# Optimization experiments

Hardware: AMD Instinct MI355X
Metric: run time of the kernel (lower is better)

The kernel has to match this reference:

```python
import jax, jax.numpy as jnp
import numpy as np

N_NODES = 100000
N_EDGES = 1600000
DIMS = [128, 128, 128, 64]


def setup_inputs() -> dict:
    key = jax.random.key(0)
    ks = jax.random.split(key, 12)
    inp = {
        "features": jax.random.normal(ks[0], (N_NODES, DIMS[0]), dtype=jnp.float32),
        "src": jax.random.randint(ks[1], (N_EDGES,), 0, N_NODES, dtype=jnp.int64),
        "dst": jax.random.randint(ks[2], (N_EDGES,), 0, N_NODES, dtype=jnp.int64),
        "edge_weight": jax.random.uniform(ks[3], (N_EDGES,), dtype=jnp.float32),
    }
    # GraphConv weights (xavier-like scale) and biases per layer
    for i in range(3):
        fin, fout = DIMS[i], DIMS[i + 1]
        scale = (2.0 / (fin + fout)) ** 0.5
        inp[f"W{i}"] = jax.random.normal(ks[4 + i], (fin, fout), dtype=jnp.float32) * scale
        inp[f"b{i}"] = jnp.zeros((fout,), dtype=jnp.float32)
    return inp


def _graph_conv(h, W, b, src, dst, ew, out_norm, in_norm):
    # DGL GraphConv, norm='both', with per-edge weight (u_mul_e message).
    fin, fout = W.shape
    h = h * out_norm[:, None]
    if fin > fout:  # mult W first to reduce message width
        h = h @ W
    msg = h[src] * ew[:, None]                       # [E, d] irregular gather
    agg = jax.ops.segment_sum(msg, dst, num_segments=N_NODES)
    agg = agg * in_norm[:, None]
    if fin <= fout:
        agg = agg @ W
    return agg + b


def reference(features, src, dst, edge_weight, W0, b0, W1, b1, W2, b2):
    ones = jnp.ones((N_EDGES,), dtype=features.dtype)
    out_deg = jax.ops.segment_sum(ones, src, num_segments=N_NODES)
    in_deg = jax.ops.segment_sum(ones, dst, num_segments=N_NODES)
    out_norm = jnp.clip(out_deg, 1.0, None) ** -0.5
    in_norm = jnp.clip(in_deg, 1.0, None) ** -0.5
    h = features
    Ws = [(W0, b0), (W1, b1), (W2, b2)]
    for i, (W, b) in enumerate(Ws):
        h = _graph_conv(h, W, b, src, dst, edge_weight, out_norm, in_norm)
        if i < len(Ws) - 1:
            h = jax.nn.relu(h)
    return h
```

## Files before the change

kernel.cpp:

```cpp
#include <hip/hip_runtime.h>
#include <cstddef>
#include <cstdint>

typedef float f4 __attribute__((ext_vector_type(4)));
typedef unsigned long long u64;
typedef unsigned short u16;
typedef unsigned short u16x8 __attribute__((ext_vector_type(8)));
typedef short short8 __attribute__((ext_vector_type(8)));

__device__ __forceinline__ u64 ldnt8(const void* p) {
    return __builtin_nontemporal_load((const u64*)(p));
}
__device__ __forceinline__ u16 bfrn(float f) {
    unsigned u = __float_as_uint(f);
    return (u16)((u + 0x7FFFu + ((u >> 16) & 1u)) >> 16);
}
__device__ __forceinline__ float bl(unsigned w) { return __uint_as_float(w << 16); }
__device__ __forceinline__ float bh(unsigned w) { return __uint_as_float(w & 0xFFFF0000u); }


#define EPB 4096

__global__ void __launch_bounds__(256)
k_p1(const int* __restrict__ src, const int* __restrict__ dst,
     u16* __restrict__ lrank_s, u16* __restrict__ lrank_d,
     int* __restrict__ bh_s, int* __restrict__ bh_d, int NB, int E) {
    __shared__ int hs[512], hd[512];
    const int t = threadIdx.x, b = blockIdx.x;
    for (int i = t; i < NB; i += 256) { hs[i] = 0; hd[i] = 0; }
    __syncthreads();
    const int e0 = b * EPB;
    #pragma unroll
    for (int j = 0; j < 4; ++j) {
        const int e = e0 + j * 1024 + t * 4;
        if (e + 4 <= E) {
            const int4 d = *(const int4*)&dst[e];
            const int4 s = *(const int4*)&src[e];
            unsigned rd0 = atomicAdd(&hd[d.x >> 8], 1);
            unsigned rd1 = atomicAdd(&hd[d.y >> 8], 1);
            unsigned rd2 = atomicAdd(&hd[d.z >> 8], 1);
            unsigned rd3 = atomicAdd(&hd[d.w >> 8], 1);
            unsigned rs0 = atomicAdd(&hs[s.x >> 8], 1);
            unsigned rs1 = atomicAdd(&hs[s.y >> 8], 1);
            unsigned rs2 = atomicAdd(&hs[s.z >> 8], 1);
            unsigned rs3 = atomicAdd(&hs[s.w >> 8], 1);
            *(uint2*)&lrank_d[e] = make_uint2(rd0 | (rd1 << 16), rd2 | (rd3 << 16));
            *(uint2*)&lrank_s[e] = make_uint2(rs0 | (rs1 << 16), rs2 | (rs3 << 16));
        } else {
            for (int k = e; k < E && k < e + 4; ++k) {
                lrank_d[k] = (u16)atomicAdd(&hd[dst[k] >> 8], 1);
                lrank_s[k] = (u16)atomicAdd(&hs[src[k] >> 8], 1);
            }
        }
    }
    __syncthreads();
    for (int i = t; i < NB; i += 256) {
        bh_d[b * NB + i] = hd[i];
        bh_s[b * NB + i] = hs[i];
    }
}

__global__ void __launch_bounds__(512)
k_p2(int* __restrict__ bh_d, int* __restrict__ bh_s,
     int* __restrict__ cb_d, int* __restrict__ cb_s, int NB, int B1) {
    __shared__ int s[512];
    const int B = blockIdx.x, i = threadIdx.x;
    int* bh = blockIdx.y ? bh_s : bh_d;
    int* cb = blockIdx.y ? cb_s : cb_d;
    const int v = (i < B1) ? bh[i * NB + B] : 0;
    s[i] = v;
    __syncthreads();
    for (int off = 1; off < 512; off <<= 1) {
        const int x = (i >= off) ? s[i - off] : 0;
        __syncthreads();
        s[i] += x;
        __syncthreads();
    }
    if (i < B1) bh[i * NB + B] = s[i] - v;
    if (i == 511) cb[B] = s[511];
}

__global__ void __launch_bounds__(512)
k_p2b(const int* __restrict__ cb_d, const int* __restrict__ cb_s,
      int* __restrict__ bktb_d, int* __restrict__ bktb_s,
      int* __restrict__ row, int NB, int N, int E) {
    __shared__ int s[512];
    const int t = threadIdx.x;
    int v = (t < NB) ? cb_d[t] : 0;
    s[t] = v;
    __syncthreads();
    for (int off = 1; off < 512; off <<= 1) {
        const int x = (t >= off) ? s[t - off] : 0;
        __syncthreads();
        s[t] += x;
        __syncthreads();
    }
    if (t < NB) bktb_d[t] = s[t] - v;
    __syncthreads();
    v = (t < NB) ? cb_s[t] : 0;
    s[t] = v;
    __syncthreads();
    for (int off = 1; off < 512; off <<= 1) {
        const int x = (t >= off) ? s[t - off] : 0;
        __syncthreads();
        s[t] += x;
        __syncthreads();
    }
    if (t < NB) bktb_s[t] = s[t] - v;
    if (t == 0) row[N] = E;
}

__global__ void __launch_bounds__(256)
k_p3(const int* __restrict__ src, const int* __restrict__ dst,
     const float* __restrict__ ew,
     const u16* __restrict__ lrank_s, const u16* __restrict__ lrank_d,
     const int* __restrict__ bh_s, const int* __restrict__ bh_d,
     const int* __restrict__ bktb_s, const int* __restrict__ bktb_d,
     int* __restrict__ tdst, int2* __restrict__ tsw, int* __restrict__ tsrc,
     int NB, int E) {
    const int t = threadIdx.x, b = blockIdx.x;
    const int e0 = b * EPB;
    #pragma unroll
    for (int j = 0; j < 4; ++j) {
        const int e = e0 + j * 1024 + t * 4;
        if (e + 4 <= E) {
            const int4 d = *(const int4*)&dst[e];
            const int4 s = *(const int4*)&src[e];
            const f4   w = *(const f4*)&ew[e];
            const uint2 rd = *(const uint2*)&lrank_d[e];
            const uint2 rs = *(const uint2*)&lrank_s[e];
            const int dd[4] = {d.x, d.y, d.z, d.w};
            const int ss[4] = {s.x, s.y, s.z, s.w};
            const float ww[4] = {w.x, w.y, w.z, w.w};
            const int rrd[4] = {(int)(rd.x & 0xFFFF), (int)(rd.x >> 16),
                                (int)(rd.y & 0xFFFF), (int)(rd.y >> 16)};
            const int rrs[4] = {(int)(rs.x & 0xFFFF), (int)(rs.x >> 16),
                                (int)(rs.y & 0xFFFF), (int)(rs.y >> 16)};
            #pragma unroll
            for (int k = 0; k < 4; ++k) {
                const int Bd = dd[k] >> 8;
                const int posd = bktb_d[Bd] + bh_d[b * NB + Bd] + rrd[k];
                tdst[posd] = dd[k];
                tsw[posd] = make_int2(ss[k], __float_as_int(ww[k]));
                const int Bs = ss[k] >> 8;
                const int poss = bktb_s[Bs] + bh_s[b * NB + Bs] + rrs[k];
                tsrc[poss] = ss[k];
            }
        } else {
            for (int k = e; k < E && k < e + 4; ++k) {
                const int dv = dst[k], sv = src[k];
                const int Bd = dv >> 8;
                const int posd = bktb_d[Bd] + bh_d[b * NB + Bd] + (int)lrank_d[k];
                tdst[posd] = dv;
                tsw[posd] = make_int2(sv, __float_as_int(ew[k]));
                const int Bs = sv >> 8;
                const int poss = bktb_s[Bs] + bh_s[b * NB + Bs] + (int)lrank_s[k];
                tsrc[poss] = sv;
            }
        }
    }
}

__global__ void __launch_bounds__(256)
k_p4s(const int* __restrict__ tsrc, const int* __restrict__ bktb_s,
      const int* __restrict__ cb_s, float* __restrict__ onorm, int NB, int N) {
    __shared__ int cnt[256];
    const int B = blockIdx.x, t = threadIdx.x;
    cnt[t] = 0;
    __syncthreads();
    const int base = bktb_s[B], cb = cb_s[B];
    for (int i = t; i < cb; i += 256) atomicAdd(&cnt[tsrc[base + i] & 255], 1);
    __syncthreads();
    const int n = (B << 8) + t;
    if (n < N) {
        const int c = cnt[t];
        onorm[n] = rsqrtf((float)(c < 1 ? 1 : c));
    }
}

__global__ void __launch_bounds__(256)
k_p4d(const int* __restrict__ tdst, const int2* __restrict__ tsw,
      const int* __restrict__ bktb_d, const int* __restrict__ cb_d,
      const float* __restrict__ onorm, int* __restrict__ row,
      float* __restrict__ inorm, int2* __restrict__ csr, int NB, int N) {
    __shared__ int cnt[256], cnt2[256], lrow[256], sc[256];
    const int B = blockIdx.x, t = threadIdx.x;
    cnt[t] = 0; cnt2[t] = 0;
    __syncthreads();
    const int base = bktb_d[B], cb = cb_d[B];
    for (int i = t; i < cb; i += 256) atomicAdd(&cnt[tdst[base + i] & 255], 1);
    __syncthreads();
    const int v = cnt[t];
    sc[t] = v;
    __syncthreads();
    for (int off = 1; off < 256; off <<= 1) {
        const int x = (t >= off) ? sc[t - off] : 0;
        __syncthreads();
        sc[t] += x;
        __syncthreads();
    }
    const int excl = sc[t] - v;
    lrow[t] = excl;
    const int n = (B << 8) + t;
    if (n < N) {
        row[n] = base + excl;
        inorm[n] = rsqrtf((float)(v < 1 ? 1 : v));
    }
    __syncthreads();
    for (int i = t; i < cb; i += 256) {
        const int d = tdst[base + i] & 255;
        const int2 sw = tsw[base + i];
        const int r = atomicAdd(&cnt2[d], 1);
        const float coef = __int_as_float(sw.y) * onorm[sw.x];
        csr[base + lrow[d] + r] = make_int2(sw.x, __float_as_int(coef));
    }
}

__global__ void __launch_bounds__(256)
k_cvt(const float* __restrict__ in, u16* __restrict__ out, int n8) {
    const int i = blockIdx.x * blockDim.x + threadIdx.x;
    if (i < n8) {
        const f4 v0 = *(const f4*)(in + (size_t)i * 8);
        const f4 v1 = *(const f4*)(in + (size_t)i * 8 + 4);
        u16x8 r = {bfrn(v0.x), bfrn(v0.y), bfrn(v0.z), bfrn(v0.w),
                   bfrn(v1.x), bfrn(v1.y), bfrn(v1.z), bfrn(v1.w)};
        *(u16x8*)(out + (size_t)i * 8) = r;
    }
}

template <int LOGC>
__global__ void __launch_bounds__(256)
k_wcvt(const float* __restrict__ W, u16* __restrict__ Wt, int K) {
    const int idx = blockIdx.x * 256 + threadIdx.x;
    if (idx < (K << LOGC)) {
        const int k = idx >> LOGC;
        const int c = idx & ((1 << LOGC) - 1);
        Wt[(size_t)c * K + k] = bfrn(W[idx]);
    }
}

__global__ void __launch_bounds__(256)
k_agg128b(const u16* __restrict__ h, const int* __restrict__ row,
          const int2* __restrict__ csr, const float* __restrict__ inorm,
          u16* __restrict__ out, int N) {
    const int node = (int)((blockIdx.x * blockDim.x + threadIdx.x) >> 6);
    if (node >= N) return;
    const int lane = threadIdx.x & 63;
    const int q = lane >> 4;
    const int col = (lane & 15) * 8;
    int p = row[node];
    const int e = row[node + 1];
    float a0 = 0, a1 = 0, a2 = 0, a3 = 0, a4 = 0, a5 = 0, a6 = 0, a7 = 0;
    for (; p + 16 <= e; p += 16) {
        const u64 c0 = ldnt8(&csr[p + q]);
        const u64 c1 = ldnt8(&csr[p + 4 + q]);
        const u64 c2 = ldnt8(&csr[p + 8 + q]);
        const u64 c3 = ldnt8(&csr[p + 12 + q]);
        const uint4 w0 = *(const uint4*)(h + (size_t)(int)c0 * 128 + col);
        const uint4 w1 = *(const uint4*)(h + (size_t)(int)c1 * 128 + col);
        const uint4 w2 = *(const uint4*)(h + (size_t)(int)c2 * 128 + col);
        const uint4 w3 = *(const uint4*)(h + (size_t)(int)c3 * 128 + col);
        const float f0 = __int_as_float((int)(c0 >> 32));
        const float f1 = __int_as_float((int)(c1 >> 32));
        const float f2 = __int_as_float((int)(c2 >> 32));
        const float f3 = __int_as_float((int)(c3 >> 32));
        a0 = fmaf(f0, bl(w0.x), a0); a1 = fmaf(f0, bh(w0.x), a1);
        a2 = fmaf(f0, bl(w0.y), a2); a3 = fmaf(f0, bh(w0.y), a3);
        a4 = fmaf(f0, bl(w0.z), a4); a5 = fmaf(f0, bh(w0.z), a5);
        a6 = fmaf(f0, bl(w0.w), a6); a7 = fmaf(f0, bh(w0.w), a7);
        a0 = fmaf(f1, bl(w1.x), a0); a1 = fmaf(f1, bh(w1.x), a1);
        a2 = fmaf(f1, bl(w1.y), a2); a3 = fmaf(f1, bh(w1.y), a3);
        a4 = fmaf(f1, bl(w1.z), a4); a5 = fmaf(f1, bh(w1.z), a5);
        a6 = fmaf(f1, bl(w1.w), a6); a7 = fmaf(f1, bh(w1.w), a7);
        a0 = fmaf(f2, bl(w2.x), a0); a1 = fmaf(f2, bh(w2.x), a1);
        a2 = fmaf(f2, bl(w2.y), a2); a3 = fmaf(f2, bh(w2.y), a3);
        a4 = fmaf(f2, bl(w2.z), a4); a5 = fmaf(f2, bh(w2.z), a5);
        a6 = fmaf(f2, bl(w2.w), a6); a7 = fmaf(f2, bh(w2.w), a7);
        a0 = fmaf(f3, bl(w3.x), a0); a1 = fmaf(f3, bh(w3.x), a1);
        a2 = fmaf(f3, bl(w3.y), a2); a3 = fmaf(f3, bh(w3.y), a3);
        a4 = fmaf(f3, bl(w3.z), a4); a5 = fmaf(f3, bh(w3.z), a5);
        a6 = fmaf(f3, bl(w3.w), a6); a7 = fmaf(f3, bh(w3.w), a7);
    }
    for (; p + 8 <= e; p += 8) {
        const u64 c0 = ldnt8(&csr[p + q]);
        const u64 c1 = ldnt8(&csr[p + 4 + q]);
        const uint4 w0 = *(const uint4*)(h + (size_t)(int)c0 * 128 + col);
        const uint4 w1 = *(const uint4*)(h + (size_t)(int)c1 * 128 + col);
        const float f0 = __int_as_float((int)(c0 >> 32));
        const float f1 = __int_as_float((int)(c1 >> 32));
        a0 = fmaf(f0, bl(w0.x), a0); a1 = fmaf(f0, bh(w0.x), a1);
        a2 = fmaf(f0, bl(w0.y), a2); a3 = fmaf(f0, bh(w0.y), a3);
        a4 = fmaf(f0, bl(w0.z), a4); a5 = fmaf(f0, bh(w0.z), a5);
        a6 = fmaf(f0, bl(w0.w), a6); a7 = fmaf(f0, bh(w0.w), a7);
        a0 = fmaf(f1, bl(w1.x), a0); a1 = fmaf(f1, bh(w1.x), a1);
        a2 = fmaf(f1, bl(w1.y), a2); a3 = fmaf(f1, bh(w1.y), a3);
        a4 = fmaf(f1, bl(w1.z), a4); a5 = fmaf(f1, bh(w1.z), a5);
        a6 = fmaf(f1, bl(w1.w), a6); a7 = fmaf(f1, bh(w1.w), a7);
    }
    {
        const int i0 = p + q, i1 = p + 4 + q;
        if (i0 < e) {
            const u64 c = ldnt8(&csr[i0]);
            const uint4 w = *(const uint4*)(h + (size_t)(int)c * 128 + col);
            const float f = __int_as_float((int)(c >> 32));
            a0 = fmaf(f, bl(w.x), a0); a1 = fmaf(f, bh(w.x), a1);
            a2 = fmaf(f, bl(w.y), a2); a3 = fmaf(f, bh(w.y), a3);
            a4 = fmaf(f, bl(w.z), a4); a5 = fmaf(f, bh(w.z), a5);
            a6 = fmaf(f, bl(w.w), a6); a7 = fmaf(f, bh(w.w), a7);
        }
        if (i1 < e) {
            const u64 c = ldnt8(&csr[i1]);
            const uint4 w = *(const uint4*)(h + (size_t)(int)c * 128 + col);
            const float f = __int_as_float((int)(c >> 32));
            a0 = fmaf(f, bl(w.x), a0); a1 = fmaf(f, bh(w.x), a1);
            a2 = fmaf(f, bl(w.y), a2); a3 = fmaf(f, bh(w.y), a3);
            a4 = fmaf(f, bl(w.z), a4); a5 = fmaf(f, bh(w.z), a5);
            a6 = fmaf(f, bl(w.w), a6); a7 = fmaf(f, bh(w.w), a7);
        }
    }
    a0 += __shfl_xor(a0, 16); a1 += __shfl_xor(a1, 16);
    a2 += __shfl_xor(a2, 16); a3 += __shfl_xor(a3, 16);
    a4 += __shfl_xor(a4, 16); a5 += __shfl_xor(a5, 16);
    a6 += __shfl_xor(a6, 16); a7 += __shfl_xor(a7, 16);
    a0 += __shfl_xor(a0, 32); a1 += __shfl_xor(a1, 32);
    a2 += __shfl_xor(a2, 32); a3 += __shfl_xor(a3, 32);
    a4 += __shfl_xor(a4, 32); a5 += __shfl_xor(a5, 32);
    a6 += __shfl_xor(a6, 32); a7 += __shfl_xor(a7, 32);
    if (lane < 16) {
        const float nn = inorm[node];
        u16x8 r = {bfrn(a0 * nn), bfrn(a1 * nn), bfrn(a2 * nn), bfrn(a3 * nn),
                   bfrn(a4 * nn), bfrn(a5 * nn), bfrn(a6 * nn), bfrn(a7 * nn)};
        *(u16x8*)(out + (size_t)node * 128 + col) = r;
    }
}

__global__ void __launch_bounds__(256)
k_agg64b(const u16* __restrict__ h, const int* __restrict__ row,
         const int2* __restrict__ csr, const float* __restrict__ inorm,
         const float* __restrict__ bias, float* __restrict__ out, int N) {
    const int node = (int)((blockIdx.x * blockDim.x + threadIdx.x) >> 6);
    if (node >= N) return;
    const int lane = threadIdx.x & 63;
    const int oc = lane >> 3;
    const int col = (lane & 7) * 8;
    int p = row[node];
    const int e = row[node + 1];
    float a0 = 0, a1 = 0, a2 = 0, a3 = 0, a4 = 0, a5 = 0, a6 = 0, a7 = 0;
    for (; p + 16 <= e; p += 16) {
        const u64 c0 = ldnt8(&csr[p + oc]);
        const u64 c1 = ldnt8(&csr[p + 8 + oc]);
        const uint4 w0 = *(const uint4*)(h + (size_t)(int)c0 * 64 + col);
        const uint4 w1 = *(const uint4*)(h + (size_t)(int)c1 * 64 + col);
        const float f0 = __int_as_float((int)(c0 >> 32));
        const float f1 = __int_as_float((int)(c1 >> 32));
        a0 = fmaf(f0, bl(w0.x), a0); a1 = fmaf(f0, bh(w0.x), a1);
        a2 = fmaf(f0, bl(w0.y), a2); a3 = fmaf(f0, bh(w0.y), a3);
        a4 = fmaf(f0, bl(w0.z), a4); a5 = fmaf(f0, bh(w0.z), a5);
        a6 = fmaf(f0, bl(w0.w), a6); a7 = fmaf(f0, bh(w0.w), a7);
        a0 = fmaf(f1, bl(w1.x), a0); a1 = fmaf(f1, bh(w1.x), a1);
        a2 = fmaf(f1, bl(w1.y), a2); a3 = fmaf(f1, bh(w1.y), a3);
        a4 = fmaf(f1, bl(w1.z), a4); a5 = fmaf(f1, bh(w1.z), a5);
        a6 = fmaf(f1, bl(w1.w), a6); a7 = fmaf(f1, bh(w1.w), a7);
    }
    {
        const int i0 = p + oc, i1 = p + 8 + oc;
        if (i0 < e) {
            const u64 c = ldnt8(&csr[i0]);
            const uint4 w = *(const uint4*)(h + (size_t)(int)c * 64 + col);
            const float f = __int_as_float((int)(c >> 32));
            a0 = fmaf(f, bl(w.x), a0); a1 = fmaf(f, bh(w.x), a1);
            a2 = fmaf(f, bl(w.y), a2); a3 = fmaf(f, bh(w.y), a3);
            a4 = fmaf(f, bl(w.z), a4); a5 = fmaf(f, bh(w.z), a5);
            a6 = fmaf(f, bl(w.w), a6); a7 = fmaf(f, bh(w.w), a7);
        }
        if (i1 < e) {
            const u64 c = ldnt8(&csr[i1]);
            const uint4 w = *(const uint4*)(h + (size_t)(int)c * 64 + col);
            const float f = __int_as_float((int)(c >> 32));
            a0 = fmaf(f, bl(w.x), a0); a1 = fmaf(f, bh(w.x), a1);
            a2 = fmaf(f, bl(w.y), a2); a3 = fmaf(f, bh(w.y), a3);
            a4 = fmaf(f, bl(w.z), a4); a5 = fmaf(f, bh(w.z), a5);
            a6 = fmaf(f, bl(w.w), a6); a7 = fmaf(f, bh(w.w), a7);
        }
    }
    a0 += __shfl_xor(a0, 8);  a1 += __shfl_xor(a1, 8);
    a2 += __shfl_xor(a2, 8);  a3 += __shfl_xor(a3, 8);
    a4 += __shfl_xor(a4, 8);  a5 += __shfl_xor(a5, 8);
    a6 += __shfl_xor(a6, 8);  a7 += __shfl_xor(a7, 8);
    a0 += __shfl_xor(a0, 16); a1 += __shfl_xor(a1, 16);
    a2 += __shfl_xor(a2, 16); a3 += __shfl_xor(a3, 16);
    a4 += __shfl_xor(a4, 16); a5 += __shfl_xor(a5, 16);
    a6 += __shfl_xor(a6, 16); a7 += __shfl_xor(a7, 16);
    a0 += __shfl_xor(a0, 32); a1 += __shfl_xor(a1, 32);
    a2 += __shfl_xor(a2, 32); a3 += __shfl_xor(a3, 32);
    a4 += __shfl_xor(a4, 32); a5 += __shfl_xor(a5, 32);
    a6 += __shfl_xor(a6, 32); a7 += __shfl_xor(a7, 32);
    if (lane < 8) {
        const float nn = inorm[node];
        const f4 b0 = *(const f4*)(bias + col);
        const f4 b1 = *(const f4*)(bias + col + 4);
        f4 r0 = {a0 * nn + b0.x, a1 * nn + b0.y, a2 * nn + b0.z, a3 * nn + b0.w};
        f4 r1 = {a4 * nn + b1.x, a5 * nn + b1.y, a6 * nn + b1.z, a7 * nn + b1.w};
        *(f4*)(out + (size_t)node * 64 + col) = r0;
        *(f4*)(out + (size_t)node * 64 + col + 4) = r1;
    }
}

template <int COLS, bool RELU, bool BIAS>
__global__ void __launch_bounds__(256)
k_mgemm(const u16* __restrict__ A, const u16* __restrict__ Wt,
        const float* __restrict__ bias, u16* __restrict__ C, int N) {
    __shared__ u16 Wl[COLS][136];
    const int t = threadIdx.x;
    const int lane = t & 63;
    const int wave = t >> 6;
    #pragma unroll
    for (int i = 0; i < COLS / 16; ++i) {
        const int elem = (i * 256 + t) * 8;
        const int r = elem >> 7, c0 = elem & 127;
        *(short8*)&Wl[r][c0] = *(const short8*)(Wt + elem);
    }
    const int row0 = blockIdx.x * 64 + wave * 16;
    const int arow = min(row0 + (lane & 15), N - 1);
    const int koff = (lane >> 4) * 8;
    short8 a[4];
    #pragma unroll
    for (int kk = 0; kk < 4; ++kk)
        a[kk] = *(const short8*)(A + (size_t)arow * 128 + kk * 32 + koff);
    __syncthreads();

    f4 acc[COLS / 16];
    #pragma unroll
    for (int ct = 0; ct < COLS / 16; ++ct) acc[ct] = (f4){0.f, 0.f, 0.f, 0.f};

    #pragma unroll
    for (int ct = 0; ct < COLS / 16; ++ct) {
        #pragma unroll
        for (int kk = 0; kk < 4; ++kk) {
            const short8 b = *(const short8*)&Wl[ct * 16 + (lane & 15)][kk * 32 + koff];
            acc[ct] = __builtin_amdgcn_mfma_f32_16x16x32_bf16(a[kk], b, acc[ct], 0, 0, 0);
        }
    }

    #pragma unroll
    for (int ct = 0; ct < COLS / 16; ++ct) {
        const int c = ct * 16 + (lane & 15);
        const float bb = BIAS ? bias[c] : 0.f;
        #pragma unroll
        for (int r = 0; r < 4; ++r) {
            const int gr = row0 + (lane >> 4) * 4 + r;
            if (gr < N) {
                float v = acc[ct][r] + bb;
                if (RELU) v = v > 0.f ? v : 0.f;
                C[(size_t)gr * COLS + c] = bfrn(v);
            }
        }
    }
}

extern "C" void kernel_launch(void* const* d_in, const int* in_sizes, int n_in,
                              void* d_out, int out_size, void* d_ws, size_t ws_size,
                              hipStream_t stream) {
    const float* feat = (const float*)d_in[0];
    const int*   src  = (const int*)d_in[1];
    const int*   dst  = (const int*)d_in[2];
    const float* ew   = (const float*)d_in[3];
    const float* W0   = (const float*)d_in[4];
    const float* b0   = (const float*)d_in[5];
    const float* W1   = (const float*)d_in[6];
    const float* b1   = (const float*)d_in[7];
    const float* W2   = (const float*)d_in[8];
    const float* b2   = (const float*)d_in[9];
    float* out = (float*)d_out;

    const int N = in_sizes[0] / 128;
    const int E = in_sizes[1];
    const int NB = (N + 255) / 256;
    const int B1 = (E + EPB - 1) / EPB;

    uint8_t* wp = (uint8_t*)d_ws;
    auto alloc = [&](size_t bytes) {
        uint8_t* r = wp;
        wp += (bytes + 511) & ~(size_t)511;
        return r;
    };
    u16*   featb = (u16*)alloc((size_t)N * 128 * 2);
    u16*   Xb    = (u16*)alloc((size_t)N * 128 * 2);
    u16*   Yb    = (u16*)alloc((size_t)N * 128 * 2 + 65536);
    int2*  csr   = (int2*)alloc((size_t)E * 8);
    int*   row   = (int*)alloc((size_t)(N + 1) * 4);
    float* onorm = (float*)alloc((size_t)N * 4);
    float* inorm = (float*)alloc((size_t)N * 4);
    u16*   Wt0   = (u16*)alloc(128 * 128 * 2);
    u16*   Wt1   = (u16*)alloc(128 * 128 * 2);
    u16*   Wt2   = (u16*)alloc(128 * 64 * 2);

    uint8_t* xp = (uint8_t*)Xb;
    auto xalloc = [&](size_t bytes) {
        uint8_t* r = xp;
        xp += (bytes + 511) & ~(size_t)511;
        return r;
    };
    u16* lrank_d = (u16*)xalloc((size_t)E * 2);
    u16* lrank_s = (u16*)xalloc((size_t)E * 2);
    int* bh_d    = (int*)xalloc((size_t)B1 * NB * 4);
    int* bh_s    = (int*)xalloc((size_t)B1 * NB * 4);
    int* cb_d    = (int*)xalloc((size_t)NB * 4);
    int* cb_s    = (int*)xalloc((size_t)NB * 4);
    int* bktb_d  = (int*)xalloc((size_t)NB * 4);
    int* bktb_s  = (int*)xalloc((size_t)NB * 4);

    uint8_t* yp = (uint8_t*)Yb;
    auto yalloc = [&](size_t bytes) {
        uint8_t* r = yp;
        yp += (bytes + 511) & ~(size_t)511;
        return r;
    };
    int*  tdst = (int*)yalloc((size_t)E * 4);
    int2* tsw  = (int2*)yalloc((size_t)E * 8);
    int*  tsrc = (int*)yalloc((size_t)E * 4);
    u16*  Gb   = (u16*)Yb;

    k_cvt<<<(N * 128 / 8 + 255) / 256, 256, 0, stream>>>(feat, featb, N * 128 / 8);
    k_wcvt<7><<<64, 256, 0, stream>>>(W0, Wt0, 128);
    k_wcvt<7><<<64, 256, 0, stream>>>(W1, Wt1, 128);
    k_wcvt<6><<<32, 256, 0, stream>>>(W2, Wt2, 128);
    k_p1<<<B1, 256, 0, stream>>>(src, dst, lrank_s, lrank_d, bh_s, bh_d, NB, E);
    k_p2<<<dim3(NB, 2), 512, 0, stream>>>(bh_d, bh_s, cb_d, cb_s, NB, B1);
    k_p2b<<<1, 512, 0, stream>>>(cb_d, cb_s, bktb_d, bktb_s, row, NB, N, E);
    k_p3<<<B1, 256, 0, stream>>>(src, dst, ew, lrank_s, lrank_d, bh_s, bh_d,
                                 bktb_s, bktb_d, tdst, tsw, tsrc, NB, E);
    k_p4s<<<NB, 256, 0, stream>>>(tsrc, bktb_s, cb_s, onorm, NB, N);
    k_p4d<<<NB, 256, 0, stream>>>(tdst, tsw, bktb_d, cb_d, onorm, row, inorm,
                                  csr, NB, N);

    const int ab = (N + 3) / 4;
    const int gb = (N + 63) / 64;

    k_agg128b<<<ab, 256, 0, stream>>>(featb, row, csr, inorm, Yb, N);
    k_mgemm<128, true, true><<<gb, 256, 0, stream>>>(Yb, Wt0, b0, Xb, N);
    k_agg128b<<<ab, 256, 0, stream>>>(Xb, row, csr, inorm, Yb, N);
    k_mgemm<128, true, true><<<gb, 256, 0, stream>>>(Yb, Wt1, b1, Xb, N);
    k_mgemm<64, false, false><<<gb, 256, 0, stream>>>(Xb, Wt2, nullptr, Gb, N);
    k_agg64b<<<ab, 256, 0, stream>>>(Gb, row, csr, inorm, b2, out, N);
}
```

Before: 338.7 us.

## Fuse aggregation with MFMA GEMM per 64-node tile, shrink sort scratch to bytes

Aggregation is now fused with the following dense layer. Each wave aggregates 16 nodes into an LDS tile and then runs bf16 MFMA against the weight matrix read from global/L2, which removes the round trip of the Y intermediate through HBM and two kernel launches. The three weight-conversion launches are merged into one. The bucket-sort scratch arrays for dst/src now hold only the low byte, cutting scatter and read traffic. The cost is lower parallelism in aggregation, since one wave now walks 16 nodes serially. The weight fragments are also no longer staged in LDS.

```diff
diff --git a/kernel.cpp b/kernel.cpp
--- a/kernel.cpp
+++ b/kernel.cpp
@@ -5,6 +5,7 @@
 typedef float f4 __attribute__((ext_vector_type(4)));
 typedef unsigned long long u64;
 typedef unsigned short u16;
+typedef unsigned char u8;
 typedef unsigned short u16x8 __attribute__((ext_vector_type(8)));
 typedef short short8 __attribute__((ext_vector_type(8)));
 
@@ -116,7 +117,7 @@
      const u16* __restrict__ lrank_s, const u16* __restrict__ lrank_d,
      const int* __restrict__ bh_s, const int* __restrict__ bh_d,
      const int* __restrict__ bktb_s, const int* __restrict__ bktb_d,
-     int* __restrict__ tdst, int2* __restrict__ tsw, int* __restrict__ tsrc,
+     u8* __restrict__ tdst, int2* __restrict__ tsw, u8* __restrict__ tsrc,
      int NB, int E) {
     const int t = threadIdx.x, b = blockIdx.x;
     const int e0 = b * EPB;
@@ -140,36 +141,36 @@
             for (int k = 0; k < 4; ++k) {
                 const int Bd = dd[k] >> 8;
                 const int posd = bktb_d[Bd] + bh_d[b * NB + Bd] + rrd[k];
-                tdst[posd] = dd[k];
+                tdst[posd] = (u8)(dd[k] & 255);
                 tsw[posd] = make_int2(ss[k], __float_as_int(ww[k]));
                 const int Bs = ss[k] >> 8;
                 const int poss = bktb_s[Bs] + bh_s[b * NB + Bs] + rrs[k];
-                tsrc[poss] = ss[k];
+                tsrc[poss] = (u8)(ss[k] & 255);
             }
         } else {
             for (int k = e; k < E && k < e + 4; ++k) {
                 const int dv = dst[k], sv = src[k];
                 const int Bd = dv >> 8;
                 const int posd = bktb_d[Bd] + bh_d[b * NB + Bd] + (int)lrank_d[k];
-                tdst[posd] = dv;
+                tdst[posd] = (u8)(dv & 255);
                 tsw[posd] = make_int2(sv, __float_as_int(ew[k]));
                 const int Bs = sv >> 8;
                 const int poss = bktb_s[Bs] + bh_s[b * NB + Bs] + (int)lrank_s[k];
-                tsrc[poss] = sv;
+                tsrc[poss] = (u8)(sv & 255);
             }
         }
     }
 }
 
 __global__ void __launch_bounds__(256)
-k_p4s(const int* __restrict__ tsrc, const int* __restrict__ bktb_s,
+k_p4s(const u8* __restrict__ tsrc, const int* __restrict__ bktb_s,
       const int* __restrict__ cb_s, float* __restrict__ onorm, int NB, int N) {
     __shared__ int cnt[256];
     const int B = blockIdx.x, t = threadIdx.x;
     cnt[t] = 0;
     __syncthreads();
     const int base = bktb_s[B], cb = cb_s[B];
-    for (int i = t; i < cb; i += 256) atomicAdd(&cnt[tsrc[base + i] & 255], 1);
+    for (int i = t; i < cb; i += 256) atomicAdd(&cnt[tsrc[base + i]], 1);
     __syncthreads();
     const int n = (B << 8) + t;
     if (n < N) {
@@ -179,7 +180,7 @@
 }
 
 __global__ void __launch_bounds__(256)
-k_p4d(const int* __restrict__ tdst, const int2* __restrict__ tsw,
+k_p4d(const u8* __restrict__ tdst, const int2* __restrict__ tsw,
       const int* __restrict__ bktb_d, const int* __restrict__ cb_d,
       const float* __restrict__ onorm, int* __restrict__ row,
       float* __restrict__ inorm, int2* __restrict__ csr, int NB, int N) {
@@ -188,7 +189,7 @@
     cnt[t] = 0; cnt2[t] = 0;
     __syncthreads();
     const int base = bktb_d[B], cb = cb_d[B];
-    for (int i = t; i < cb; i += 256) atomicAdd(&cnt[tdst[base + i] & 255], 1);
+    for (int i = t; i < cb; i += 256) atomicAdd(&cnt[tdst[base + i]], 1);
     __syncthreads();
     const int v = cnt[t];
     sc[t] = v;
@@ -208,7 +209,7 @@
     }
     __syncthreads();
     for (int i = t; i < cb; i += 256) {
-        const int d = tdst[base + i] & 255;
+        const int d = tdst[base + i];
         const int2 sw = tsw[base + i];
         const int r = atomicAdd(&cnt2[d], 1);
         const float coef = __int_as_float(sw.y) * onorm[sw.x];
@@ -228,109 +229,179 @@
     }
 }
 
-template <int LOGC>
-__global__ void __launch_bounds__(256)
-k_wcvt(const float* __restrict__ W, u16* __restrict__ Wt, int K) {
-    const int idx = blockIdx.x * 256 + threadIdx.x;
-    if (idx < (K << LOGC)) {
-        const int k = idx >> LOGC;
-        const int c = idx & ((1 << LOGC) - 1);
-        Wt[(size_t)c * K + k] = bfrn(W[idx]);
-    }
-}
-
-__global__ void __launch_bounds__(256)
-k_agg128b(const u16* __restrict__ h, const int* __restrict__ row,
-          const int2* __restrict__ csr, const float* __restrict__ inorm,
-          u16* __restrict__ out, int N) {
-    const int node = (int)((blockIdx.x * blockDim.x + threadIdx.x) >> 6);
-    if (node >= N) return;
-    const int lane = threadIdx.x & 63;
-    const int q = lane >> 4;
-    const int col = (lane & 15) * 8;
-    int p = row[node];
-    const int e = row[node + 1];
-    float a0 = 0, a1 = 0, a2 = 0, a3 = 0, a4 = 0, a5 = 0, a6 = 0, a7 = 0;
-    for (; p + 16 <= e; p += 16) {
-        const u64 c0 = ldnt8(&csr[p + q]);
-        const u64 c1 = ldnt8(&csr[p + 4 + q]);
-        const u64 c2 = ldnt8(&csr[p + 8 + q]);
-        const u64 c3 = ldnt8(&csr[p + 12 + q]);
-        const uint4 w0 = *(const uint4*)(h + (size_t)(int)c0 * 128 + col);
-        const uint4 w1 = *(const uint4*)(h + (size_t)(int)c1 * 128 + col);
-        const uint4 w2 = *(const uint4*)(h + (size_t)(int)c2 * 128 + col);
-        const uint4 w3 = *(const uint4*)(h + (size_t)(int)c3 * 128 + col);
-        const float f0 = __int_as_float((int)(c0 >> 32));
-        const float f1 = __int_as_float((int)(c1 >> 32));
-        const float f2 = __int_as_float((int)(c2 >> 32));
-        const float f3 = __int_as_float((int)(c3 >> 32));
-        a0 = fmaf(f0, bl(w0.x), a0); a1 = fmaf(f0, bh(w0.x), a1);
-        a2 = fmaf(f0, bl(w0.y), a2); a3 = fmaf(f0, bh(w0.y), a3);
-        a4 = fmaf(f0, bl(w0.z), a4); a5 = fmaf(f0, bh(w0.z), a5);
-        a6 = fmaf(f0, bl(w0.w), a6); a7 = fmaf(f0, bh(w0.w), a7);
-        a0 = fmaf(f1, bl(w1.x), a0); a1 = fmaf(f1, bh(w1.x), a1);
-        a2 = fmaf(f1, bl(w1.y), a2); a3 = fmaf(f1, bh(w1.y), a3);
-        a4 = fmaf(f1, bl(w1.z), a4); a5 = fmaf(f1, bh(w1.z), a5);
-        a6 = fmaf(f1, bl(w1.w), a6); a7 = fmaf(f1, bh(w1.w), a7);
-        a0 = fmaf(f2, bl(w2.x), a0); a1 = fmaf(f2, bh(w2.x), a1);
-        a2 = fmaf(f2, bl(w2.y), a2); a3 = fmaf(f2, bh(w2.y), a3);
-        a4 = fmaf(f2, bl(w2.z), a4); a5 = fmaf(f2, bh(w2.z), a5);
-        a6 = fmaf(f2, bl(w2.w), a6); a7 = fmaf(f2, bh(w2.w), a7);
-        a0 = fmaf(f3, bl(w3.x), a0); a1 = fmaf(f3, bh(w3.x), a1);
-        a2 = fmaf(f3, bl(w3.y), a2); a3 = fmaf(f3, bh(w3.y), a3);
-        a4 = fmaf(f3, bl(w3.z), a4); a5 = fmaf(f3, bh(w3.z), a5);
-        a6 = fmaf(f3, bl(w3.w), a6); a7 = fmaf(f3, bh(w3.w), a7);
-    }
-    for (; p + 8 <= e; p += 8) {
-        const u64 c0 = ldnt8(&csr[p + q]);
-        const u64 c1 = ldnt8(&csr[p + 4 + q]);
-        const uint4 w0 = *(const uint4*)(h + (size_t)(int)c0 * 128 + col);
-        const uint4 w1 = *(const uint4*)(h + (size_t)(int)c1 * 128 + col);
-        const float f0 = __int_as_float((int)(c0 >> 32));
-        const float f1 = __int_as_float((int)(c1 >> 32));
-        a0 = fmaf(f0, bl(w0.x), a0); a1 = fmaf(f0, bh(w0.x), a1);
-        a2 = fmaf(f0, bl(w0.y), a2); a3 = fmaf(f0, bh(w0.y), a3);
-        a4 = fmaf(f0, bl(w0.z), a4); a5 = fmaf(f0, bh(w0.z), a5);
-        a6 = fmaf(f0, bl(w0.w), a6); a7 = fmaf(f0, bh(w0.w), a7);
-        a0 = fmaf(f1, bl(w1.x), a0); a1 = fmaf(f1, bh(w1.x), a1);
-        a2 = fmaf(f1, bl(w1.y), a2); a3 = fmaf(f1, bh(w1.y), a3);
-        a4 = fmaf(f1, bl(w1.z), a4); a5 = fmaf(f1, bh(w1.z), a5);
-        a6 = fmaf(f1, bl(w1.w), a6); a7 = fmaf(f1, bh(w1.w), a7);
-    }
-    {
-        const int i0 = p + q, i1 = p + 4 + q;
-        if (i0 < e) {
-            const u64 c = ldnt8(&csr[i0]);
-            const uint4 w = *(const uint4*)(h + (size_t)(int)c * 128 + col);
-            const float f = __int_as_float((int)(c >> 32));
-            a0 = fmaf(f, bl(w.x), a0); a1 = fmaf(f, bh(w.x), a1);
-            a2 = fmaf(f, bl(w.y), a2); a3 = fmaf(f, bh(w.y), a3);
-            a4 = fmaf(f, bl(w.z), a4); a5 = fmaf(f, bh(w.z), a5);
-            a6 = fmaf(f, bl(w.w), a6); a7 = fmaf(f, bh(w.w), a7);
-        }
-        if (i1 < e) {
-            const u64 c = ldnt8(&csr[i1]);
-            const uint4 w = *(const uint4*)(h + (size_t)(int)c * 128 + col);
-            const float f = __int_as_float((int)(c >> 32));
-            a0 = fmaf(f, bl(w.x), a0); a1 = fmaf(f, bh(w.x), a1);
-            a2 = fmaf(f, bl(w.y), a2); a3 = fmaf(f, bh(w.y), a3);
-            a4 = fmaf(f, bl(w.z), a4); a5 = fmaf(f, bh(w.z), a5);
-            a6 = fmaf(f, bl(w.w), a6); a7 = fmaf(f, bh(w.w), a7);
-        }
-    }
-    a0 += __shfl_xor(a0, 16); a1 += __shfl_xor(a1, 16);
-    a2 += __shfl_xor(a2, 16); a3 += __shfl_xor(a3, 16);
-    a4 += __shfl_xor(a4, 16); a5 += __shfl_xor(a5, 16);
-    a6 += __shfl_xor(a6, 16); a7 += __shfl_xor(a7, 16);
-    a0 += __shfl_xor(a0, 32); a1 += __shfl_xor(a1, 32);
-    a2 += __shfl_xor(a2, 32); a3 += __shfl_xor(a3, 32);
-    a4 += __shfl_xor(a4, 32); a5 += __shfl_xor(a5, 32);
-    a6 += __shfl_xor(a6, 32); a7 += __shfl_xor(a7, 32);
-    if (lane < 16) {
-        const float nn = inorm[node];
-        u16x8 r = {bfrn(a0 * nn), bfrn(a1 * nn), bfrn(a2 * nn), bfrn(a3 * nn),
-                   bfrn(a4 * nn), bfrn(a5 * nn), bfrn(a6 * nn), bfrn(a7 * nn)};
-        *(u16x8*)(out + (size_t)node * 128 + col) = r;
+__global__ void __launch_bounds__(256)
+k_wcvt3(const float* __restrict__ W0, const float* __restrict__ W1,
+        const float* __restrict__ W2, u16* __restrict__ Wt0,
+        u16* __restrict__ Wt1, u16* __restrict__ Wt2) {
+    const int i = blockIdx.x * 256 + threadIdx.x;
+    if (i < 16384) {
+        const int k = i >> 7, c = i & 127;
+        Wt0[c * 128 + k] = bfrn(W0[i]);
+    } else if (i < 32768) {
+        const int j = i - 16384, k = j >> 7, c = j & 127;
+        Wt1[c * 128 + k] = bfrn(W1[j]);
+    } else if (i < 40960) {
+        const int j = i - 32768, k = j >> 6, c = j & 63;
+        Wt2[c * 128 + k] = bfrn(W2[j]);
+    }
+}
+
+template <bool RELU>
+__global__ void __launch_bounds__(256, 8)
+k_aggemm(const u16* __restrict__ h, const int* __restrict__ row,
+         const int2* __restrict__ csr, const float* __restrict__ inorm,
+         const u16* __restrict__ Wt, const float* __restrict__ bias,
+         u16* __restrict__ C, int N) {
+    __shared__ u16 Yt[64][136];
+    const int t = threadIdx.x, lane = t & 63, wave = t >> 6;
+    const int q = lane >> 4, col = (lane & 15) * 8;
+    const int nbase = blockIdx.x * 64 + wave * 16;
+
+    int rv = 0;
+    if (lane <= 16) rv = row[min(nbase + lane, N)];
+
+    for (int i = 0; i < 16; ++i) {
+        const int node = nbase + i;
+        if (node >= N) break;
+        int p = __shfl(rv, i);
+        const int e = __shfl(rv, i + 1);
+        float a0 = 0, a1 = 0, a2 = 0, a3 = 0, a4 = 0, a5 = 0, a6 = 0, a7 = 0;
+        for (; p + 16 <= e; p += 16) {
+            const u64 c0 = ldnt8(&csr[p + q]);
+            const u64 c1 = ldnt8(&csr[p + 4 + q]);
+            const u64 c2 = ldnt8(&csr[p + 8 + q]);
+            const u64 c3 = ldnt8(&csr[p + 12 + q]);
+            const uint4 w0 = *(const uint4*)(h + (size_t)(int)c0 * 128 + col);
+            const uint4 w1 = *(const uint4*)(h + (size_t)(int)c1 * 128 + col);
+            const uint4 w2 = *(const uint4*)(h + (size_t)(int)c2 * 128 + col);
+            const uint4 w3 = *(const uint4*)(h + (size_t)(int)c3 * 128 + col);
+            const float f0 = __int_as_float((int)(c0 >> 32));
+            const float f1 = __int_as_float((int)(c1 >> 32));
+            const float f2 = __int_as_float((int)(c2 >> 32));
+            const float f3 = __int_as_float((int)(c3 >> 32));
+            a0 = fmaf(f0, bl(w0.x), a0); a1 = fmaf(f0, bh(w0.x), a1);
+            a2 = fmaf(f0, bl(w0.y), a2); a3 = fmaf(f0, bh(w0.y), a3);
+            a4 = fmaf(f0, bl(w0.z), a4); a5 = fmaf(f0, bh(w0.z), a5);
+            a6 = fmaf(f0, bl(w0.w), a6); a7 = fmaf(f0, bh(w0.w), a7);
+            a0 = fmaf(f1, bl(w1.x), a0); a1 = fmaf(f1, bh(w1.x), a1);
+            a2 = fmaf(f1, bl(w1.y), a2); a3 = fmaf(f1, bh(w1.y), a3);
+            a4 = fmaf(f1, bl(w1.z), a4); a5 = fmaf(f1, bh(w1.z), a5);
+            a6 = fmaf(f1, bl(w1.w), a6); a7 = fmaf(f1, bh(w1.w), a7);
+            a0 = fmaf(f2, bl(w2.x), a0); a1 = fmaf(f2, bh(w2.x), a1);
+            a2 = fmaf(f2, bl(w2.y), a2); a3 = fmaf(f2, bh(w2.y), a3);
+            a4 = fmaf(f2, bl(w2.z), a4); a5 = fmaf(f2, bh(w2.z), a5);
+            a6 = fmaf(f2, bl(w2.w), a6); a7 = fmaf(f2, bh(w2.w), a7);
+            a0 = fmaf(f3, bl(w3.x), a0); a1 = fmaf(f3, bh(w3.x), a1);
+            a2 = fmaf(f3, bl(w3.y), a2); a3 = fmaf(f3, bh(w3.y), a3);
+            a4 = fmaf(f3, bl(w3.z), a4); a5 = fmaf(f3, bh(w3.z), a5);
+            a6 = fmaf(f3, bl(w3.w), a6); a7 = fmaf(f3, bh(w3.w), a7);
+        }
+        for (; p + 8 <= e; p += 8) {
+            const u64 c0 = ldnt8(&csr[p + q]);
+            const u64 c1 = ldnt8(&csr[p + 4 + q]);
+            const uint4 w0 = *(const uint4*)(h + (size_t)(int)c0 * 128 + col);
+            const uint4 w1 = *(const uint4*)(h + (size_t)(int)c1 * 128 + col);
+            const float f0 = __int_as_float((int)(c0 >> 32));
+            const float f1 = __int_as_float((int)(c1 >> 32));
+            a0 = fmaf(f0, bl(w0.x), a0); a1 = fmaf(f0, bh(w0.x), a1);
+            a2 = fmaf(f0, bl(w0.y), a2); a3 = fmaf(f0, bh(w0.y), a3);
+            a4 = fmaf(f0, bl(w0.z), a4); a5 = fmaf(f0, bh(w0.z), a5);
+            a6 = fmaf(f0, bl(w0.w), a6); a7 = fmaf(f0, bh(w0.w), a7);
+            a0 = fmaf(f1, bl(w1.x), a0); a1 = fmaf(f1, bh(w1.x), a1);
+            a2 = fmaf(f1, bl(w1.y), a2); a3 = fmaf(f1, bh(w1.y), a3);
+            a4 = fmaf(f1, bl(w1.z), a4); a5 = fmaf(f1, bh(w1.z), a5);
+            a6 = fmaf(f1, bl(w1.w), a6); a7 = fmaf(f1, bh(w1.w), a7);
+        }
+        {
+            const int i0 = p + q, i1 = p + 4 + q;
+            if (i0 < e) {
+                const u64 c = ldnt8(&csr[i0]);
+                const uint4 w = *(const uint4*)(h + (size_t)(int)c * 128 + col);
+                const float f = __int_as_float((int)(c >> 32));
+                a0 = fmaf(f, bl(w.x), a0); a1 = fmaf(f, bh(w.x), a1);
+                a2 = fmaf(f, bl(w.y), a2); a3 = fmaf(f, bh(w.y), a3);
+                a4 = fmaf(f, bl(w.z), a4); a5 = fmaf(f, bh(w.z), a5);
+                a6 = fmaf(f, bl(w.w), a6); a7 = fmaf(f, bh(w.w), a7);
+            }
+            if (i1 < e) {
+                const u64 c = ldnt8(&csr[i1]);
+                const uint4 w = *(const uint4*)(h + (size_t)(int)c * 128 + col);
+                const float f = __int_as_float((int)(c >> 32));
+                a0 = fmaf(f, bl(w.x), a0); a1 = fmaf(f, bh(w.x), a1);
+                a2 = fmaf(f, bl(w.y), a2); a3 = fmaf(f, bh(w.y), a3);
+                a4 = fmaf(f, bl(w.z), a4); a5 = fmaf(f, bh(w.z), a5);
+                a6 = fmaf(f, bl(w.w), a6); a7 = fmaf(f, bh(w.w), a7);
+            }
+        }
+        a0 += __shfl_xor(a0, 16); a1 += __shfl_xor(a1, 16);
+        a2 += __shfl_xor(a2, 16); a3 += __shfl_xor(a3, 16);
+        a4 += __shfl_xor(a4, 16); a5 += __shfl_xor(a5, 16);
+        a6 += __shfl_xor(a6, 16); a7 += __shfl_xor(a7, 16);
+        a0 += __shfl_xor(a0, 32); a1 += __shfl_xor(a1, 32);
+        a2 += __shfl_xor(a2, 32); a3 += __shfl_xor(a3, 32);
+        a4 += __shfl_xor(a4, 32); a5 += __shfl_xor(a5, 32);
+        a6 += __shfl_xor(a6, 32); a7 += __shfl_xor(a7, 32);
+        if (lane < 16) {
+            const float nn = inorm[node];
+            u16x8 r = {bfrn(a0 * nn), bfrn(a1 * nn), bfrn(a2 * nn), bfrn(a3 * nn),
+                       bfrn(a4 * nn), bfrn(a5 * nn), bfrn(a6 * nn), bfrn(a7 * nn)};
+            *(u16x8*)&Yt[wave * 16 + i][col] = r;
+        }
+    }
+
+    const int c16 = lane & 15;
+    const int koff = q * 8;
+    short8 a[4];
+    #pragma unroll
+    for (int kk = 0; kk < 4; ++kk)
+        a[kk] = *(const short8*)&Yt[wave * 16 + c16][kk * 32 + koff];
+
+    #pragma unroll
+    for (int ct = 0; ct < 8; ++ct) {
+        f4 acc = {0.f, 0.f, 0.f, 0.f};
+        #pragma unroll
+        for (int kk = 0; kk < 4; ++kk) {
+            const short8 b = *(const short8*)(Wt + (size_t)(ct * 16 + c16) * 128 + kk * 32 + koff);
+            acc = __builtin_amdgcn_mfma_f32_16x16x32_bf16(a[kk], b, acc, 0, 0, 0);
+        }
+        const float bb = bias[ct * 16 + c16];
+        #pragma unroll
+        for (int r = 0; r < 4; ++r) {
+            const int gr = nbase + q * 4 + r;
+            if (gr < N) {
+                float v = acc[r] + bb;
+                if (RELU) v = v > 0.f ? v : 0.f;
+                C[(size_t)gr * 128 + ct * 16 + c16] = bfrn(v);
+            }
+        }
+    }
+}
+
+__global__ void __launch_bounds__(256, 8)
+k_mgemm64(const u16* __restrict__ A, const u16* __restrict__ Wt,
+          u16* __restrict__ C, int N) {
+    const int t = threadIdx.x, lane = t & 63, wave = t >> 6;
+    const int q = lane >> 4, c16 = lane & 15, koff = q * 8;
+    const int row0 = blockIdx.x * 64 + wave * 16;
+    if (row0 >= N) return;
+    const int arow = min(row0 + c16, N - 1);
+    short8 a[4];
+    #pragma unroll
+    for (int kk = 0; kk < 4; ++kk)
+        a[kk] = *(const short8*)(A + (size_t)arow * 128 + kk * 32 + koff);
+    #pragma unroll
+    for (int ct = 0; ct < 4; ++ct) {
+        f4 acc = {0.f, 0.f, 0.f, 0.f};
+        #pragma unroll
+        for (int kk = 0; kk < 4; ++kk) {
+            const short8 b = *(const short8*)(Wt + (size_t)(ct * 16 + c16) * 128 + kk * 32 + koff);
+            acc = __builtin_amdgcn_mfma_f32_16x16x32_bf16(a[kk], b, acc, 0, 0, 0);
+        }
+        #pragma unroll
+        for (int r = 0; r < 4; ++r) {
+            const int gr = row0 + q * 4 + r;
+            if (gr < N) C[(size_t)gr * 64 + ct * 16 + c16] = bfrn(acc[r]);
+        }
     }
 }
 
@@ -406,58 +477,6 @@
     }
 }
 
-template <int COLS, bool RELU, bool BIAS>
-__global__ void __launch_bounds__(256)
-k_mgemm(const u16* __restrict__ A, const u16* __restrict__ Wt,
-        const float* __restrict__ bias, u16* __restrict__ C, int N) {
-    __shared__ u16 Wl[COLS][136];
-    const int t = threadIdx.x;
-    const int lane = t & 63;
-    const int wave = t >> 6;
-    #pragma unroll
-    for (int i = 0; i < COLS / 16; ++i) {
-        const int elem = (i * 256 + t) * 8;
-        const int r = elem >> 7, c0 = elem & 127;
-        *(short8*)&Wl[r][c0] = *(const short8*)(Wt + elem);
-    }
-    const int row0 = blockIdx.x * 64 + wave * 16;
-    const int arow = min(row0 + (lane & 15), N - 1);
-    const int koff = (lane >> 4) * 8;
-    short8 a[4];
-    #pragma unroll
-    for (int kk = 0; kk < 4; ++kk)
-        a[kk] = *(const short8*)(A + (size_t)arow * 128 + kk * 32 + koff);
-    __syncthreads();
-
-    f4 acc[COLS / 16];
-    #pragma unroll
-    for (int ct = 0; ct < COLS / 16; ++ct) acc[ct] = (f4){0.f, 0.f, 0.f, 0.f};
-
-    #pragma unroll
-    for (int ct = 0; ct < COLS / 16; ++ct) {
-        #pragma unroll
-        for (int kk = 0; kk < 4; ++kk) {
-            const short8 b = *(const short8*)&Wl[ct * 16 + (lane & 15)][kk * 32 + koff];
-            acc[ct] = __builtin_amdgcn_mfma_f32_16x16x32_bf16(a[kk], b, acc[ct], 0, 0, 0);
-        }
-    }
-
-    #pragma unroll
-    for (int ct = 0; ct < COLS / 16; ++ct) {
-        const int c = ct * 16 + (lane & 15);
-        const float bb = BIAS ? bias[c] : 0.f;
-        #pragma unroll
-        for (int r = 0; r < 4; ++r) {
-            const int gr = row0 + (lane >> 4) * 4 + r;
-            if (gr < N) {
-                float v = acc[ct][r] + bb;
-                if (RELU) v = v > 0.f ? v : 0.f;
-                C[(size_t)gr * COLS + c] = bfrn(v);
-            }
-        }
-    }
-}
-
 extern "C" void kernel_launch(void* const* d_in, const int* in_sizes, int n_in,
                               void* d_out, int out_size, void* d_ws, size_t ws_size,
                               hipStream_t stream) {
@@ -486,7 +505,7 @@
     };
     u16*   featb = (u16*)alloc((size_t)N * 128 * 2);
     u16*   Xb    = (u16*)alloc((size_t)N * 128 * 2);
-    u16*   Yb    = (u16*)alloc((size_t)N * 128 * 2 + 65536);
+    u8*    scr   = (u8*)alloc((size_t)E * 16 + 65536);
     int2*  csr   = (int2*)alloc((size_t)E * 8);
     int*   row   = (int*)alloc((size_t)(N + 1) * 4);
     float* onorm = (float*)alloc((size_t)N * 4);
@@ -510,21 +529,19 @@
     int* bktb_d  = (int*)xalloc((size_t)NB * 4);
     int* bktb_s  = (int*)xalloc((size_t)NB * 4);
 
-    uint8_t* yp = (uint8_t*)Yb;
+    uint8_t* yp = scr;
     auto yalloc = [&](size_t bytes) {
         uint8_t* r = yp;
         yp += (bytes + 511) & ~(size_t)511;
         return r;
     };
-    int*  tdst = (int*)yalloc((size_t)E * 4);
+    u8*   tdst = (u8*)yalloc((size_t)E);
     int2* tsw  = (int2*)yalloc((size_t)E * 8);
-    int*  tsrc = (int*)yalloc((size_t)E * 4);
-    u16*  Gb   = (u16*)Yb;
+    u8*   tsrc = (u8*)yalloc((size_t)E);
+    u16*  Gb   = (u16*)scr;
 
     k_cvt<<<(N * 128 / 8 + 255) / 256, 256, 0, stream>>>(feat, featb, N * 128 / 8);
-    k_wcvt<7><<<64, 256, 0, stream>>>(W0, Wt0, 128);
-    k_wcvt<7><<<64, 256, 0, stream>>>(W1, Wt1, 128);
-    k_wcvt<6><<<32, 256, 0, stream>>>(W2, Wt2, 128);
+    k_wcvt3<<<160, 256, 0, stream>>>(W0, W1, W2, Wt0, Wt1, Wt2);
     k_p1<<<B1, 256, 0, stream>>>(src, dst, lrank_s, lrank_d, bh_s, bh_d, NB, E);
     k_p2<<<dim3(NB, 2), 512, 0, stream>>>(bh_d, bh_s, cb_d, cb_s, NB, B1);
     k_p2b<<<1, 512, 0, stream>>>(cb_d, cb_s, bktb_d, bktb_s, row, NB, N, E);
@@ -534,13 +551,11 @@
     k_p4d<<<NB, 256, 0, stream>>>(tdst, tsw, bktb_d, cb_d, onorm, row, inorm,
                                   csr, NB, N);
 
+    const int fb = (N + 63) / 64;
     const int ab = (N + 3) / 4;
-    const int gb = (N + 63) / 64;
-
-    k_agg128b<<<ab, 256, 0, stream>>>(featb, row, csr, inorm, Yb, N);
-    k_mgemm<128, true, true><<<gb, 256, 0, stream>>>(Yb, Wt0, b0, Xb, N);
-    k_agg128b<<<ab, 256, 0, stream>>>(Xb, row, csr, inorm, Yb, N);
-    k_mgemm<128, true, true><<<gb, 256, 0, stream>>>(Yb, Wt1, b1, Xb, N);
-    k_mgemm<64, false, false><<<gb, 256, 0, stream>>>(Xb, Wt2, nullptr, Gb, N);
+
+    k_aggemm<true><<<fb, 256, 0, stream>>>(featb, row, csr, inorm, Wt0, b0, Xb, N);
+    k_aggemm<true><<<fb, 256, 0, stream>>>(Xb, row, csr, inorm, Wt1, b1, featb, N);
+    k_mgemm64<<<fb, 256, 0, stream>>>(featb, Wt2, Gb, N);
     k_agg64b<<<ab, 256, 0, stream>>>(Gb, row, csr, inorm, b2, out, N);
 }
```

New measurement: 353.0 us. 1.04x slower.
